# Optimization experiments

Hardware: AMD Instinct MI355X
Metric: run time of the kernel (lower is better)

The kernel has to match this reference:

```python
import jax, jax.numpy as jnp
import numpy as np

SCENE = (128, 128, 8)      # (X, Y, Z) voxel grid
VOXEL_SIZE = 0.4
DOWNSAMPLE_Z = 2
NUM_HEADS = 8
NUM_POINTS = 4
LN_EPS = 1e-5


def _pix2vox(depth, K, E, voxel_origin):
    # depth [1,H,W]; K [1,3,3]; E [1,4,4]; voxel_origin [1,3]
    B, H, W = depth.shape
    gx, gy = jnp.meshgrid(jnp.arange(W, dtype=depth.dtype), jnp.arange(H, dtype=depth.dtype))
    pix = jnp.stack([gx, gy])                              # [2,H,W] -> (u, v) after flip in torch
    d = depth[:, None]                                     # [B,1,H,W]
    p_x = jnp.concatenate([pix[None] * d, d], 1).reshape(B, 3, -1)
    p_c = jnp.linalg.inv(K) @ p_x                          # camera coords [B,3,HW]
    p_c = jnp.concatenate([p_c, jnp.ones_like(p_c[:, :1])], 1)
    p_w = jnp.linalg.inv(E) @ p_c                          # world coords [B,4,HW]
    p_v = (jnp.swapaxes(p_w[:, :3], 1, 2) - voxel_origin[:, None, :]) / VOXEL_SIZE - 0.5
    p_v = p_v.at[..., 2].set(p_v[..., 2] / DOWNSAMPLE_Z)
    return jnp.trunc(p_v).astype(jnp.int32)               # torch .long() truncates toward 0


def _voxel_mask(p_v):
    X, Y, Z = SCENE
    p = p_v[0]                                             # [HW,3] (batch asserted == 1)
    valid = ((p[:, 0] >= 0) & (p[:, 0] < X) & (p[:, 1] >= 0) & (p[:, 1] < Y)
             & (p[:, 2] >= 0) & (p[:, 2] < Z))
    flat = jnp.where(valid, (p[:, 0] * Y + p[:, 1]) * Z + p[:, 2], 0)
    return jnp.zeros(X * Y * Z, dtype=bool).at[flat].max(valid)


def _ms_deform_attn(q, feats, ref, Wv, bv, Woff, boff, Wattw, battw, Wout, bout):
    # q [N,C]; feats: list of [C,Hl,Wl]; ref [N,2] normalized (shared across levels)
    N, C = q.shape
    hd = C // NUM_HEADS
    shapes = [(f.shape[1], f.shape[2]) for f in feats]
    L = len(feats)
    flat = jnp.concatenate([f.reshape(C, -1).T for f in feats], 0)      # [Lsum, C]
    value = (flat @ Wv.T + bv).reshape(-1, NUM_HEADS, hd)               # [Lsum, h, hd]
    off = (q @ Woff.T + boff).reshape(N, NUM_HEADS, L, NUM_POINTS, 2)
    w = jax.nn.softmax((q @ Wattw.T + battw).reshape(N, NUM_HEADS, L * NUM_POINTS), -1)
    w = w.reshape(N, NUM_HEADS, L, NUM_POINTS)
    normalizer = jnp.array([[wl, hl] for (hl, wl) in shapes], dtype=q.dtype)  # (W,H) per level
    loc = ref[:, None, None, None, :] + off / normalizer[None, None, :, None, :]
    h_idx = jnp.arange(NUM_HEADS)[None, :, None]
    out = jnp.zeros((N, NUM_HEADS, hd), q.dtype)
    start = 0
    for lvl, (Hl, Wl) in enumerate(shapes):
        v = value[start:start + Hl * Wl]                   # [Hl*Wl, h, hd]
        start += Hl * Wl
        # grid_sample bilinear, align_corners=False, zero padding
        x = loc[:, :, lvl, :, 0] * Wl - 0.5                # [N,h,P]
        y = loc[:, :, lvl, :, 1] * Hl - 0.5
        x0 = jnp.floor(x); y0 = jnp.floor(y)
        lx = x - x0; ly = y - y0
        x0i = x0.astype(jnp.int32); y0i = y0.astype(jnp.int32)
        samp = jnp.zeros((N, NUM_HEADS, NUM_POINTS, hd), q.dtype)
        for dy, dx, wgt in ((0, 0, (1 - lx) * (1 - ly)), (0, 1, lx * (1 - ly)),
                            (1, 0, (1 - lx) * ly), (1, 1, lx * ly)):
            xi = x0i + dx; yi = y0i + dy
            ok = (xi >= 0) & (xi < Wl) & (yi >= 0) & (yi < Hl)
            idx = jnp.where(ok, yi * Wl + xi, 0)
            g = v[idx, h_idx]                              # [N,h,P,hd] per-head gather
            samp = samp + g * (wgt * ok)[..., None]
        out = out + jnp.einsum('nhp,nhpd->nhd', w[:, :, lvl], samp)
    return out.reshape(N, C) @ Wout.T + bout


def _forward(scene_embed, feat0, feat1, feat2, depth, K, E, voxel_origin, ref_pix,
             Wv, bv, Woff, boff, Wattw, battw, Wout, bout, ln_g, ln_b):
    X, Y, Z = SCENE
    mask = _voxel_mask(_pix2vox(depth, K, E, voxel_origin))             # [N] bool
    q = scene_embed[0]                                                  # [N,C]
    attn = _ms_deform_attn(q, [feat0[0], feat1[0], feat2[0]], ref_pix[0],
                           Wv, bv, Woff, boff, Wattw, battw, Wout, bout)
    h = q + attn                                                        # residual (MSDeformAttn identity)
    mu = jnp.mean(h, -1, keepdims=True)
    var = jnp.mean((h - mu) ** 2, -1, keepdims=True)
    h = (h - mu) / jnp.sqrt(var + LN_EPS) * ln_g + ln_b                 # post-norm
    out = jnp.where(mask[:, None], h, q)                                # index_fov_back_to_voxels
    return out.T.reshape(1, -1, X, Y, Z)                                # nlc -> nchw [1,C,X,Y,Z]


def setup_inputs() -> dict:
    key = jax.random.key(0)
    ks = jax.random.split(key, 12)
    X, Y, Z = SCENE
    N = X * Y * Z
    C = 128
    H, W = 192, 640
    s = 0.02
    scene_embed = jax.random.normal(ks[0], (1, N, C), jnp.float32)
    feat0 = jax.random.normal(ks[1], (1, C, 48, 160), jnp.float32)
    feat1 = jax.random.normal(ks[2], (1, C, 24, 80), jnp.float32)
    feat2 = jax.random.normal(ks[3], (1, C, 12, 40), jnp.float32)
    depth = jax.random.uniform(ks[4], (1, H, W), jnp.float32, 1.0, 40.0)
    K = jnp.array([[[552.55, 0.0, 320.0], [0.0, 552.55, 96.0], [0.0, 0.0, 1.0]]], jnp.float32)
    E = jnp.eye(4, dtype=jnp.float32)[None]
    voxel_origin = jnp.array([[-25.6, -3.2, 0.0]], jnp.float32)
    ref_pix = jax.random.uniform(ks[5], (1, N, 2), jnp.float32)
    return {
        'scene_embed': scene_embed, 'feat0': feat0, 'feat1': feat1, 'feat2': feat2,
        'depth': depth, 'K': K, 'E': E, 'voxel_origin': voxel_origin, 'ref_pix': ref_pix,
        'Wv': jax.random.normal(ks[6], (C, C), jnp.float32) * s,
        'bv': jnp.zeros((C,), jnp.float32),
        'Woff': jax.random.normal(ks[7], (NUM_HEADS * 3 * NUM_POINTS * 2, C), jnp.float32) * s,
        'boff': jnp.zeros((NUM_HEADS * 3 * NUM_POINTS * 2,), jnp.float32),
        'Wattw': jax.random.normal(ks[8], (NUM_HEADS * 3 * NUM_POINTS, C), jnp.float32) * s,
        'battw': jnp.zeros((NUM_HEADS * 3 * NUM_POINTS,), jnp.float32),
        'Wout': jax.random.normal(ks[9], (C, C), jnp.float32) * s,
        'bout': jnp.zeros((C,), jnp.float32),
        'ln_g': jnp.ones((C,), jnp.float32),
        'ln_b': jnp.zeros((C,), jnp.float32),
    }


def reference(scene_embed, feat0, feat1, feat2, depth, K, E, voxel_origin, ref_pix,
              Wv, bv, Woff, boff, Wattw, battw, Wout, bout, ln_g, ln_b):
    return _forward(scene_embed, feat0, feat1, feat2, depth, K, E, voxel_origin, ref_pix,
                    Wv, bv, Woff, boff, Wattw, battw, Wout, bout, ln_g, ln_b)
```

## Files before the change

kernel.cpp:

```cpp
#include <hip/hip_runtime.h>
#include <hip/hip_bf16.h>
#include <stdint.h>

#define XS 128
#define YS 128
#define ZS 8
#define NQ (XS*YS*ZS)
#define CDIM 128
#define NH 8
#define HD 16
#define DH 192
#define DW 640
#define NPIX (DH*DW)
#define NVPIX 10080

typedef float f32x4 __attribute__((ext_vector_type(4)));
typedef short s16x8 __attribute__((ext_vector_type(8)));
typedef unsigned int u32x4 __attribute__((ext_vector_type(4)));

__device__ __forceinline__ float b2f(unsigned short u){
    union { unsigned int i; float f; } v; v.i = ((unsigned int)u) << 16; return v.f;
}
__device__ __forceinline__ unsigned short f2b(float f){
    __hip_bfloat16 h = __float2bfloat16(f);
    return *reinterpret_cast<unsigned short*>(&h);
}
__device__ __forceinline__ float blo(unsigned int u){
    union { unsigned int i; float f; } v; v.i = u << 16; return v.f;
}
__device__ __forceinline__ float bhi(unsigned int u){
    union { unsigned int i; float f; } v; v.i = u & 0xffff0000u; return v.f;
}

__global__ __launch_bounds__(256)
void prep_kernel(int nW, int nVal,
                 const float* __restrict__ Woff,
                 const float* __restrict__ Wattw,
                 const float* __restrict__ Wout,
                 unsigned short* __restrict__ Wbf,
                 const float* __restrict__ f0,
                 const float* __restrict__ f1,
                 const float* __restrict__ f2,
                 const float* __restrict__ Wv,
                 const float* __restrict__ bv,
                 unsigned short* __restrict__ value,
                 const float* __restrict__ depth,
                 const float* __restrict__ K,
                 const float* __restrict__ E,
                 const float* __restrict__ vorigin,
                 unsigned char* __restrict__ mask){
    __shared__ __align__(16) unsigned char smem[16384];
    const int t = threadIdx.x;

    if ((int)blockIdx.x < nW){
        int idx = blockIdx.x*256 + t;
        if (idx < 24576)      Wbf[idx] = f2b(Woff[idx]);
        else if (idx < 36864) Wbf[idx] = f2b(Wattw[idx-24576]);
        else if (idx < 40960) Wbf[idx] = 0;
        else if (idx < 57344) Wbf[idx] = f2b(Wout[idx-40960]);
    } else if ((int)blockIdx.x < nW + nVal){
        const int half = t >> 7, tt = t & 127;
        const int p0 = (blockIdx.x - nW)*8 + half*4;
        float (*fl)[4] = (float(*)[4])(smem + half*2048);
        const float* src; int hw, lp;
        if (p0 < 7680)      { src=f0; hw=7680; lp=p0; }
        else if (p0 < 9600) { src=f1; hw=1920; lp=p0-7680; }
        else                { src=f2; hw=480;  lp=p0-9600; }
        float4 v = *(const float4*)(src + tt*hw + lp);
        fl[tt][0]=v.x; fl[tt][1]=v.y; fl[tt][2]=v.z; fl[tt][3]=v.w;
        __syncthreads();
        float bb = bv[tt];
        float acc[4] = {bb,bb,bb,bb};
        const float4* wrow = (const float4*)(Wv + tt*CDIM);
        #pragma unroll 8
        for (int kc=0; kc<32; ++kc){
            float4 w = wrow[kc];
            #pragma unroll
            for (int u=0;u<4;u++){
                float wu = (u==0)?w.x:(u==1)?w.y:(u==2)?w.z:w.w;
                float4 fv = *(const float4*)fl[kc*4+u];
                acc[0] += fv.x*wu; acc[1] += fv.y*wu; acc[2] += fv.z*wu; acc[3] += fv.w*wu;
            }
        }
        const int hh = tt >> 4, cc = tt & 15;
        #pragma unroll
        for (int i=0;i<4;i++)
            value[((size_t)hh*NVPIX + (size_t)(p0+i))*HD + cc] = f2b(acc[i]);
    } else {
        double* invs = (double*)smem;
        if (t == 0){
            double k[3][3], e[4][4];
            for (int i=0;i<9;i++)  k[i/3][i%3] = (double)K[i];
            for (int i=0;i<16;i++) e[i/4][i%4] = (double)E[i];
            double det = k[0][0]*(k[1][1]*k[2][2]-k[1][2]*k[2][1])
                       - k[0][1]*(k[1][0]*k[2][2]-k[1][2]*k[2][0])
                       + k[0][2]*(k[1][0]*k[2][1]-k[1][1]*k[2][0]);
            double id = 1.0/det;
            invs[0]=(k[1][1]*k[2][2]-k[1][2]*k[2][1])*id;
            invs[1]=(k[0][2]*k[2][1]-k[0][1]*k[2][2])*id;
            invs[2]=(k[0][1]*k[1][2]-k[0][2]*k[1][1])*id;
            invs[3]=(k[1][2]*k[2][0]-k[1][0]*k[2][2])*id;
            invs[4]=(k[0][0]*k[2][2]-k[0][2]*k[2][0])*id;
            invs[5]=(k[0][2]*k[1][0]-k[0][0]*k[1][2])*id;
            invs[6]=(k[1][0]*k[2][1]-k[1][1]*k[2][0])*id;
            invs[7]=(k[0][1]*k[2][0]-k[0][0]*k[2][1])*id;
            invs[8]=(k[0][0]*k[1][1]-k[0][1]*k[1][0])*id;
            double a[4][8];
            for (int i=0;i<4;i++){ for(int j=0;j<4;j++){ a[i][j]=e[i][j]; a[i][4+j]=(i==j)?1.0:0.0; } }
            for (int c=0;c<4;c++){
                int piv=c; double best=fabs(a[c][c]);
                for (int r=c+1;r<4;r++){ double v=fabs(a[r][c]); if (v>best){best=v;piv=r;} }
                if (piv!=c){ for (int j=0;j<8;j++){ double tmp=a[c][j]; a[c][j]=a[piv][j]; a[piv][j]=tmp; } }
                double pv = 1.0/a[c][c];
                for (int j=0;j<8;j++) a[c][j]*=pv;
                for (int r=0;r<4;r++){
                    if (r==c) continue;
                    double f=a[r][c];
                    for(int j=0;j<8;j++) a[r][j]-=f*a[c][j];
                }
            }
            for (int i=0;i<12;i++) invs[9+i] = a[i/4][4 + (i%4)];
        }
        __syncthreads();
        int tid = ((int)blockIdx.x - nW - nVal)*256 + t;
        if (tid >= NPIX) return;
        int gx = tid % DW, gy = tid / DW;
        double d  = (double)depth[tid];
        double X0 = (double)gx * d, X1 = (double)gy * d, X2 = d;
        double c0 = invs[0]*X0 + invs[1]*X1 + invs[2]*X2;
        double c1 = invs[3]*X0 + invs[4]*X1 + invs[5]*X2;
        double c2 = invs[6]*X0 + invs[7]*X1 + invs[8]*X2;
        const double* iE = invs + 9;
        double w0 = iE[0]*c0 + iE[1]*c1 + iE[2]*c2  + iE[3];
        double w1 = iE[4]*c0 + iE[5]*c1 + iE[6]*c2  + iE[7];
        double w2 = iE[8]*c0 + iE[9]*c1 + iE[10]*c2 + iE[11];
        double v0 = (w0-(double)vorigin[0])/0.4 - 0.5;
        double v1 = (w1-(double)vorigin[1])/0.4 - 0.5;
        double v2 = ((w2-(double)vorigin[2])/0.4 - 0.5) / 2.0;
        int xi = (int)v0, yi = (int)v1, zi = (int)v2;
        if (xi>=0 && xi<XS && yi>=0 && yi<YS && zi>=0 && zi<ZS)
            mask[(xi*YS + yi)*ZS + zi] = 1;
    }
}

__global__ __launch_bounds__(256, 2)
void attn_fused(const float* __restrict__ q_in,
                const float* __restrict__ refpix,
                const unsigned short* __restrict__ Wbf,
                const float* __restrict__ boff,
                const float* __restrict__ battw,
                const unsigned short* __restrict__ value,
                const unsigned short* __restrict__ WoutBf,
                const float* __restrict__ bout,
                const float* __restrict__ lng,
                const float* __restrict__ lnb,
                const unsigned char* __restrict__ mask,
                float* __restrict__ dout){
    const int nq0 = blockIdx.x * 32;
    const int t = threadIdx.x;
    __shared__ __align__(16) unsigned char smem[36384];
    unsigned short* Ob    = (unsigned short*)smem;
    unsigned char*  qbfB  = smem + 18432;
    unsigned char*  descB = smem + 18432;
    float*          out2  = (float*)(smem + 18432);
    unsigned char*  obfB  = smem + 30720;
    float*          bias  = (float*)(smem + 34816);
    float*          rp_s  = (float*)(smem + 35968);
    unsigned char*  mask_s= smem + 36224;
    float*          wredp = (float*)(smem + 36256);

    #pragma unroll
    for (int i=0;i<4;i++){
        int idx = t + i*256;
        int row = idx >> 5, c4 = idx & 31;
        float4 qv = ((const float4*)(q_in + (size_t)(nq0+row)*CDIM))[c4];
        unsigned int pk0 = (unsigned int)f2b(qv.x) | ((unsigned int)f2b(qv.y)<<16);
        unsigned int pk1 = (unsigned int)f2b(qv.z) | ((unsigned int)f2b(qv.w)<<16);
        unsigned int bo = ((unsigned int)(row*256 + c4*8)) ^ (unsigned int)((row&7)<<4);
        *(unsigned int*)(qbfB + bo)     = pk0;
        *(unsigned int*)(qbfB + bo + 4) = pk1;
    }
    for (int i=t;i<288;i+=256) bias[i] = (i<192)? boff[i] : battw[i-192];
    ((unsigned int*)obfB)[512 + t] = 0;
    ((unsigned int*)obfB)[768 + t] = 0;
    if (t < 64) rp_s[t] = refpix[nq0*2 + t];
    if (t < 32) mask_s[t] = mask[nq0 + t];
    __syncthreads();

    {
        const int w = t >> 6, lane = t & 63, lr = lane & 15, lg = lane >> 4;
        const int nt0 = w*5;
        f32x4 acc[5][2];
        #pragma unroll
        for (int j=0;j<5;j++){ acc[j][0]=(f32x4){0,0,0,0}; acc[j][1]=(f32x4){0,0,0,0}; }
        #pragma unroll
        for (int ks=0; ks<4; ++ks){
            s16x8 bf[2];
            #pragma unroll
            for (int qt=0;qt<2;qt++){
                int qrow = qt*16 + lr;
                unsigned int bo = ((unsigned int)(qrow*256 + ks*64 + lg*16)) ^ (unsigned int)((qrow&7)<<4);
                bf[qt] = *(const s16x8*)(qbfB + bo);
            }
            const unsigned short* wp = Wbf + (size_t)(nt0*16 + lr)*CDIM + ks*32 + lg*8;
            #pragma unroll
            for (int j=0;j<5;++j){
                s16x8 af = *(const s16x8*)(wp + j*16*CDIM);
                acc[j][0] = __builtin_amdgcn_mfma_f32_16x16x32_bf16(af, bf[0], acc[j][0], 0, 0, 0);
                acc[j][1] = __builtin_amdgcn_mfma_f32_16x16x32_bf16(af, bf[1], acc[j][1], 0, 0, 0);
            }
        }
        #pragma unroll
        for (int j=0;j<5;++j){
            int nt = nt0 + j;
            if (nt < 18){
                #pragma unroll
                for (int qt=0;qt<2;qt++){
                    int q = qt*16 + lr;
                    int base = (q>>3)*2304 + (q&7);
                    #pragma unroll
                    for (int r=0;r<4;++r){
                        int f = nt*16 + lg*4 + r;
                        Ob[base + f*8] = f2b(acc[j][qt][r] + bias[f]);
                    }
                }
            }
        }
    }
    __syncthreads();

    {
        int q = t >> 3, h = t & 7;
        unsigned short* p = Ob + (q>>3)*2304 + (192 + h*12)*8 + (q&7);
        float e[12]; float m = -1e30f;
        #pragma unroll
        for (int i=0;i<12;i++){ e[i] = b2f(p[i*8]); m = fmaxf(m, e[i]); }
        float s = 0.f;
        #pragma unroll
        for (int i=0;i<12;i++){ e[i] = __expf(e[i]-m); s += e[i]; }
        float is = 1.f/s;
        #pragma unroll
        for (int i=0;i<12;i++) p[i*8] = f2b(e[i]*is);
    }
    __syncthreads();

    for (int sr = 0; sr < 4; ++sr){
        const unsigned short* raw = Ob + sr*2304;
        const int nsr = nq0 + sr*8;

        for (int idx = t; idx < 768; idx += 256){
            int q = idx & 7, hp = idx >> 3;
            int lp = hp % 12;
            float fw, fh; int Wl, Hl, st;
            if (lp < 4)      { fw=160.f; fh=48.f; Wl=160; Hl=48; st=0; }
            else if (lp < 8) { fw=80.f;  fh=24.f; Wl=80;  Hl=24; st=7680; }
            else             { fw=40.f;  fh=12.f; Wl=40;  Hl=12; st=9600; }
            float offx = b2f(raw[(hp*2)*8 + q]);
            float offy = b2f(raw[(hp*2+1)*8 + q]);
            float aw   = b2f(raw[(192+hp)*8 + q]);
            float x = rp_s[(sr*8+q)*2+0]*fw - 0.5f + offx;
            float y = rp_s[(sr*8+q)*2+1]*fh - 0.5f + offy;
            float x0f = floorf(x), y0f = floorf(y);
            float lx = x-x0f, ly = y-y0f;
            int x0 = (int)x0f, y0 = (int)y0f;
            bool x0ok = (x0>=0)&&(x0<Wl), x1ok=(x0+1>=0)&&(x0+1<Wl);
            bool y0ok = (y0>=0)&&(y0<Hl), y1ok=(y0+1>=0)&&(y0+1<Hl);
            float w00 = (x0ok&&y0ok)? (1.f-lx)*(1.f-ly)*aw : 0.f;
            float w01 = (x1ok&&y0ok)? lx*(1.f-ly)*aw       : 0.f;
            float w10 = (x0ok&&y1ok)? (1.f-lx)*ly*aw       : 0.f;
            float w11 = (x1ok&&y1ok)? lx*ly*aw             : 0.f;
            int yc0 = min(max(y0,0),Hl-1), yc1 = min(max(y0+1,0),Hl-1);
            int xc0 = min(max(x0,0),Wl-1), xc1 = min(max(x0+1,0),Wl-1);
            unsigned int rb0 = (unsigned int)(st + yc0*Wl), rb1 = (unsigned int)(st + yc1*Wl);
            uint4 d;
            d.x = (rb0+(unsigned int)xc0) | ((rb0+(unsigned int)xc1)<<16);
            d.y = (rb1+(unsigned int)xc0) | ((rb1+(unsigned int)xc1)<<16);
            d.z = (unsigned int)f2b(w00) | ((unsigned int)f2b(w01)<<16);
            d.w = (unsigned int)f2b(w10) | ((unsigned int)f2b(w11)<<16);
            *(uint4*)(descB + (((unsigned int)(idx ^ ((idx>>5)&7)))<<4)) = d;
        }
        __syncthreads();

        float qv[4];
        {
            const int r = t & 127, qb = t >> 7;
            #pragma unroll
            for (int qi4=0;qi4<4;qi4++)
                qv[qi4] = q_in[(size_t)(nsr + qb*4 + qi4)*CDIM + r];
        }

        {
            const int cs  = t & 1;
            const int cp2 = (t >> 1) & 1;
            const int hs  = (t >> 2) & 7;
            const int qq  = t >> 5;
            const unsigned int vbase = (unsigned int)hs*(NVPIX*HD*2) + (unsigned int)cp2*16;
            const char* vb = (const char*)value;
            float a8[8] = {0.f,0.f,0.f,0.f,0.f,0.f,0.f,0.f};
            #pragma unroll
            for (int lp=0; lp<12; ++lp){
                int idx = (hs*12+lp)*8 + qq;
                uint4 d = *(const uint4*)(descB + (((unsigned int)(idx ^ ((idx>>5)&7)))<<4));
                unsigned int pidx = cs ? d.y : d.x;
                unsigned int wpk  = cs ? d.w : d.z;
                unsigned int oa = vbase + ((pidx & 0xffffu)<<5);
                unsigned int ob = vbase + ((pidx >> 16)<<5);
                u32x4 ua = *(const u32x4*)(vb + oa);
                u32x4 ub = *(const u32x4*)(vb + ob);
                float wa = blo(wpk), wb = bhi(wpk);
                #pragma unroll
                for (int j=0;j<4;j++){
                    a8[2*j]   += blo(ua[j])*wa + blo(ub[j])*wb;
                    a8[2*j+1] += bhi(ua[j])*wa + bhi(ub[j])*wb;
                }
            }
            #pragma unroll
            for (int j=0;j<8;j++) a8[j] += __shfl_xor(a8[j], 1, 64);
            if (cs == 0){
                u32x4 pk;
                pk[0] = (unsigned int)f2b(a8[0]) | ((unsigned int)f2b(a8[1])<<16);
                pk[1] = (unsigned int)f2b(a8[2]) | ((unsigned int)f2b(a8[3])<<16);
                pk[2] = (unsigned int)f2b(a8[4]) | ((unsigned int)f2b(a8[5])<<16);
                pk[3] = (unsigned int)f2b(a8[6]) | ((unsigned int)f2b(a8[7])<<16);
                unsigned int bo = ((unsigned int)(qq*256 + hs*32 + cp2*16)) ^ (unsigned int)((qq&7)<<4);
                *(u32x4*)(obfB + bo) = pk;
            }
        }
        __syncthreads();

        {
            const int w = t >> 6, lane = t & 63, lr = lane & 15, lg = lane >> 4;
            f32x4 a0 = (f32x4){0.f,0.f,0.f,0.f};
            f32x4 a1 = (f32x4){0.f,0.f,0.f,0.f};
            #pragma unroll
            for (int ks=0; ks<4; ++ks){
                unsigned int bo = (unsigned int)(lr*256 + ks*64 + lg*16) ^ (unsigned int)((lr&7)<<4);
                s16x8 bfrag = *(const s16x8*)(obfB + bo);
                const unsigned short* wp = WoutBf + (size_t)(w*32 + lr)*CDIM + ks*32 + lg*8;
                s16x8 af0 = *(const s16x8*)(wp);
                s16x8 af1 = *(const s16x8*)(wp + 16*CDIM);
                a0 = __builtin_amdgcn_mfma_f32_16x16x32_bf16(af0, bfrag, a0, 0, 0, 0);
                a1 = __builtin_amdgcn_mfma_f32_16x16x32_bf16(af1, bfrag, a1, 0, 0, 0);
            }
            if (lr < 8){
                int f0 = w*32 + lg*4;
                float4 b0 = *(const float4*)(bout + f0);
                float4 b1 = *(const float4*)(bout + f0 + 16);
                float4 v0, v1;
                v0.x = a0[0]+b0.x; v0.y = a0[1]+b0.y; v0.z = a0[2]+b0.z; v0.w = a0[3]+b0.w;
                v1.x = a1[0]+b1.x; v1.y = a1[1]+b1.y; v1.z = a1[2]+b1.z; v1.w = a1[3]+b1.w;
                *(float4*)(out2 + lr*CDIM + f0)      = v0;
                *(float4*)(out2 + lr*CDIM + f0 + 16) = v1;
            }
        }
        __syncthreads();

        {
            const int r = t & 127;
            const int qb = t >> 7;
            const int wv = t >> 6;
            float hv[4], s1[4], s2[4];
            #pragma unroll
            for (int qi4=0;qi4<4;qi4++){
                hv[qi4] = qv[qi4] + out2[(qb*4+qi4)*CDIM + r];
                s1[qi4] = hv[qi4];
                s2[qi4] = hv[qi4]*hv[qi4];
            }
            #pragma unroll
            for (int off=32; off>0; off>>=1){
                #pragma unroll
                for (int qi4=0;qi4<4;qi4++){
                    s1[qi4] += __shfl_xor(s1[qi4], off, 64);
                    s2[qi4] += __shfl_xor(s2[qi4], off, 64);
                }
            }
            if ((t&63)==0){
                #pragma unroll
                for (int qi4=0;qi4<4;qi4++){
                    wredp[0*16 + wv*4 + qi4] = s1[qi4];
                    wredp[1*16 + wv*4 + qi4] = s2[qi4];
                }
            }
            __syncthreads();

            float res[4];
            const float g = lng[r], b = lnb[r];
            #pragma unroll
            for (int qi4=0;qi4<4;qi4++){
                float mu  = (wredp[0*16 + (qb*2)*4 + qi4] + wredp[0*16 + (qb*2+1)*4 + qi4]) * (1.f/128.f);
                float msq = (wredp[1*16 + (qb*2)*4 + qi4] + wredp[1*16 + (qb*2+1)*4 + qi4]) * (1.f/128.f);
                float var = msq - mu*mu;
                float nv  = (hv[qi4]-mu) * __frsqrt_rn(var + 1e-5f) * g + b;
                res[qi4] = mask_s[sr*8 + qb*4+qi4] ? nv : qv[qi4];
            }
            float4 o; o.x=res[0]; o.y=res[1]; o.z=res[2]; o.w=res[3];
            *(float4*)(dout + (size_t)r*NQ + nsr + qb*4) = o;
        }
        __syncthreads();
    }
}

extern "C" void kernel_launch(void* const* d_in, const int* in_sizes, int n_in,
                              void* d_out, int out_size, void* d_ws, size_t ws_size,
                              hipStream_t stream){
    const float* scene  = (const float*)d_in[0];
    const float* f0     = (const float*)d_in[1];
    const float* f1     = (const float*)d_in[2];
    const float* f2     = (const float*)d_in[3];
    const float* depth  = (const float*)d_in[4];
    const float* K      = (const float*)d_in[5];
    const float* E      = (const float*)d_in[6];
    const float* vorig  = (const float*)d_in[7];
    const float* refpix = (const float*)d_in[8];
    const float* Wv     = (const float*)d_in[9];
    const float* bv     = (const float*)d_in[10];
    const float* Woff   = (const float*)d_in[11];
    const float* boff   = (const float*)d_in[12];
    const float* Wattw  = (const float*)d_in[13];
    const float* battw  = (const float*)d_in[14];
    const float* Wout   = (const float*)d_in[15];
    const float* bout   = (const float*)d_in[16];
    const float* lng    = (const float*)d_in[17];
    const float* lnb    = (const float*)d_in[18];

    char* ws = (char*)d_ws;
    unsigned char*  mask   = (unsigned char*)(ws + 512);
    unsigned short* value  = (unsigned short*)(ws + 512 + 131072);
    unsigned short* Wbf    = (unsigned short*)(ws + 512 + 131072 + 2580480);
    unsigned short* WoutBf = Wbf + 40960;

    hipMemsetAsync(mask, 0, NQ, stream);

    int nW    = 57344/256;
    int nVal  = NVPIX/8;
    int nMask = (NPIX+255)/256;
    prep_kernel<<<nW + nVal + nMask, 256, 0, stream>>>(
        nW, nVal, Woff, Wattw, Wout, Wbf,
        f0, f1, f2, Wv, bv, value,
        depth, K, E, vorig, mask);
    attn_fused<<<NQ/32, 256, 0, stream>>>(scene, refpix, Wbf, boff, battw, value,
                                          WoutBf, bout, lng, lnb, mask,
                                          (float*)d_out);
}
```

Baseline: 402.1 us.

## Halve queries per block and remap bilinear gather threads for higher occupancy

The fused attention kernel now handles 16 queries per block instead of 32, doubling the grid, shrinking shared memory, and raising the launch-bounds occupancy hint from 2 to 6 blocks per CU. The first MFMA projection drops its second query tile, which cuts accumulator registers. The value-gather stage is remapped so each thread loads 4-byte channel pairs for two queries across all four bilinear corners, replacing 16-byte loads plus a shuffle reduction. This aims at more latency hiding for the random gathers, at the cost of narrower memory accesses and more per-block overhead such as reloading the weights.

```diff
diff --git a/kernel.cpp b/kernel.cpp
--- a/kernel.cpp
+++ b/kernel.cpp
@@ -16,7 +16,6 @@
 
 typedef float f32x4 __attribute__((ext_vector_type(4)));
 typedef short s16x8 __attribute__((ext_vector_type(8)));
-typedef unsigned int u32x4 __attribute__((ext_vector_type(4)));
 
 __device__ __forceinline__ float b2f(unsigned short u){
     union { unsigned int i; float f; } v; v.i = ((unsigned int)u) << 16; return v.f;
@@ -143,7 +142,7 @@
     }
 }
 
-__global__ __launch_bounds__(256, 2)
+__global__ __launch_bounds__(256, 6)
 void attn_fused(const float* __restrict__ q_in,
                 const float* __restrict__ refpix,
                 const unsigned short* __restrict__ Wbf,
@@ -156,21 +155,21 @@
                 const float* __restrict__ lnb,
                 const unsigned char* __restrict__ mask,
                 float* __restrict__ dout){
-    const int nq0 = blockIdx.x * 32;
+    const int nq0 = blockIdx.x * 16;
     const int t = threadIdx.x;
-    __shared__ __align__(16) unsigned char smem[36384];
+    __shared__ __align__(16) unsigned char smem[27024];
     unsigned short* Ob    = (unsigned short*)smem;
-    unsigned char*  qbfB  = smem + 18432;
-    unsigned char*  descB = smem + 18432;
-    float*          out2  = (float*)(smem + 18432);
-    unsigned char*  obfB  = smem + 30720;
-    float*          bias  = (float*)(smem + 34816);
-    float*          rp_s  = (float*)(smem + 35968);
-    unsigned char*  mask_s= smem + 36224;
-    float*          wredp = (float*)(smem + 36256);
+    unsigned char*  qbfB  = smem + 9216;
+    unsigned char*  descB = smem + 9216;
+    float*          out2  = (float*)(smem + 9216);
+    unsigned char*  obfB  = smem + 21504;
+    float*          bias  = (float*)(smem + 25600);
+    float*          rp_s  = (float*)(smem + 26752);
+    unsigned char*  mask_s= smem + 26880;
+    float*          wredp = (float*)(smem + 26896);
 
     #pragma unroll
-    for (int i=0;i<4;i++){
+    for (int i=0;i<2;i++){
         int idx = t + i*256;
         int row = idx >> 5, c4 = idx & 31;
         float4 qv = ((const float4*)(q_in + (size_t)(nq0+row)*CDIM))[c4];
@@ -183,53 +182,43 @@
     for (int i=t;i<288;i+=256) bias[i] = (i<192)? boff[i] : battw[i-192];
     ((unsigned int*)obfB)[512 + t] = 0;
     ((unsigned int*)obfB)[768 + t] = 0;
-    if (t < 64) rp_s[t] = refpix[nq0*2 + t];
-    if (t < 32) mask_s[t] = mask[nq0 + t];
+    if (t < 32) rp_s[t] = refpix[nq0*2 + t];
+    if (t < 16) mask_s[t] = mask[nq0 + t];
     __syncthreads();
 
     {
         const int w = t >> 6, lane = t & 63, lr = lane & 15, lg = lane >> 4;
         const int nt0 = w*5;
-        f32x4 acc[5][2];
-        #pragma unroll
-        for (int j=0;j<5;j++){ acc[j][0]=(f32x4){0,0,0,0}; acc[j][1]=(f32x4){0,0,0,0}; }
+        f32x4 acc[5];
+        #pragma unroll
+        for (int j=0;j<5;j++) acc[j]=(f32x4){0,0,0,0};
         #pragma unroll
         for (int ks=0; ks<4; ++ks){
-            s16x8 bf[2];
-            #pragma unroll
-            for (int qt=0;qt<2;qt++){
-                int qrow = qt*16 + lr;
-                unsigned int bo = ((unsigned int)(qrow*256 + ks*64 + lg*16)) ^ (unsigned int)((qrow&7)<<4);
-                bf[qt] = *(const s16x8*)(qbfB + bo);
-            }
+            unsigned int bo = ((unsigned int)(lr*256 + ks*64 + lg*16)) ^ (unsigned int)((lr&7)<<4);
+            s16x8 bfrag = *(const s16x8*)(qbfB + bo);
             const unsigned short* wp = Wbf + (size_t)(nt0*16 + lr)*CDIM + ks*32 + lg*8;
             #pragma unroll
             for (int j=0;j<5;++j){
                 s16x8 af = *(const s16x8*)(wp + j*16*CDIM);
-                acc[j][0] = __builtin_amdgcn_mfma_f32_16x16x32_bf16(af, bf[0], acc[j][0], 0, 0, 0);
-                acc[j][1] = __builtin_amdgcn_mfma_f32_16x16x32_bf16(af, bf[1], acc[j][1], 0, 0, 0);
+                acc[j] = __builtin_amdgcn_mfma_f32_16x16x32_bf16(af, bfrag, acc[j], 0, 0, 0);
             }
         }
         #pragma unroll
         for (int j=0;j<5;++j){
             int nt = nt0 + j;
             if (nt < 18){
+                int base = (lr>>3)*2304 + (lr&7);
                 #pragma unroll
-                for (int qt=0;qt<2;qt++){
-                    int q = qt*16 + lr;
-                    int base = (q>>3)*2304 + (q&7);
-                    #pragma unroll
-                    for (int r=0;r<4;++r){
-                        int f = nt*16 + lg*4 + r;
-                        Ob[base + f*8] = f2b(acc[j][qt][r] + bias[f]);
-                    }
+                for (int r=0;r<4;++r){
+                    int f = nt*16 + lg*4 + r;
+                    Ob[base + f*8] = f2b(acc[j][r] + bias[f]);
                 }
             }
         }
     }
     __syncthreads();
 
-    {
+    if (t < 128){
         int q = t >> 3, h = t & 7;
         unsigned short* p = Ob + (q>>3)*2304 + (192 + h*12)*8 + (q&7);
         float e[12]; float m = -1e30f;
@@ -244,7 +233,7 @@
     }
     __syncthreads();
 
-    for (int sr = 0; sr < 4; ++sr){
+    for (int sr = 0; sr < 2; ++sr){
         const unsigned short* raw = Ob + sr*2304;
         const int nsr = nq0 + sr*8;
 
@@ -290,41 +279,38 @@
         }
 
         {
-            const int cs  = t & 1;
-            const int cp2 = (t >> 1) & 1;
-            const int hs  = (t >> 2) & 7;
-            const int qq  = t >> 5;
-            const unsigned int vbase = (unsigned int)hs*(NVPIX*HD*2) + (unsigned int)cp2*16;
+            const int cp = t & 7, hs = (t>>3) & 7, qgs = t >> 6;
+            const unsigned int vbase = (unsigned int)hs*(NVPIX*HD*2) + (unsigned int)cp*4;
             const char* vb = (const char*)value;
-            float a8[8] = {0.f,0.f,0.f,0.f,0.f,0.f,0.f,0.f};
+            float av0x=0.f, av0y=0.f, av1x=0.f, av1y=0.f;
             #pragma unroll
             for (int lp=0; lp<12; ++lp){
-                int idx = (hs*12+lp)*8 + qq;
-                uint4 d = *(const uint4*)(descB + (((unsigned int)(idx ^ ((idx>>5)&7)))<<4));
-                unsigned int pidx = cs ? d.y : d.x;
-                unsigned int wpk  = cs ? d.w : d.z;
-                unsigned int oa = vbase + ((pidx & 0xffffu)<<5);
-                unsigned int ob = vbase + ((pidx >> 16)<<5);
-                u32x4 ua = *(const u32x4*)(vb + oa);
-                u32x4 ub = *(const u32x4*)(vb + ob);
-                float wa = blo(wpk), wb = bhi(wpk);
                 #pragma unroll
-                for (int j=0;j<4;j++){
-                    a8[2*j]   += blo(ua[j])*wa + blo(ub[j])*wb;
-                    a8[2*j+1] += bhi(ua[j])*wa + bhi(ub[j])*wb;
+                for (int qi2=0; qi2<2; ++qi2){
+                    int idx = (hs*12+lp)*8 + qgs*2 + qi2;
+                    uint4 d = *(const uint4*)(descB + (((unsigned int)(idx ^ ((idx>>5)&7)))<<4));
+                    unsigned int o00 = vbase + ((d.x & 0xffffu)<<5);
+                    unsigned int o01 = vbase + ((d.x >> 16)<<5);
+                    unsigned int o10 = vbase + ((d.y & 0xffffu)<<5);
+                    unsigned int o11 = vbase + ((d.y >> 16)<<5);
+                    unsigned int u00 = *(const unsigned int*)(vb + o00);
+                    unsigned int u01 = *(const unsigned int*)(vb + o01);
+                    unsigned int u10 = *(const unsigned int*)(vb + o10);
+                    unsigned int u11 = *(const unsigned int*)(vb + o11);
+                    float w00 = blo(d.z), w01 = bhi(d.z), w10 = blo(d.w), w11 = bhi(d.w);
+                    float sx = blo(u00)*w00 + blo(u01)*w01 + blo(u10)*w10 + blo(u11)*w11;
+                    float sy = bhi(u00)*w00 + bhi(u01)*w01 + bhi(u10)*w10 + bhi(u11)*w11;
+                    if (qi2 == 0){ av0x += sx; av0y += sy; }
+                    else         { av1x += sx; av1y += sy; }
                 }
             }
-            #pragma unroll
-            for (int j=0;j<8;j++) a8[j] += __shfl_xor(a8[j], 1, 64);
-            if (cs == 0){
-                u32x4 pk;
-                pk[0] = (unsigned int)f2b(a8[0]) | ((unsigned int)f2b(a8[1])<<16);
-                pk[1] = (unsigned int)f2b(a8[2]) | ((unsigned int)f2b(a8[3])<<16);
-                pk[2] = (unsigned int)f2b(a8[4]) | ((unsigned int)f2b(a8[5])<<16);
-                pk[3] = (unsigned int)f2b(a8[6]) | ((unsigned int)f2b(a8[7])<<16);
-                unsigned int bo = ((unsigned int)(qq*256 + hs*32 + cp2*16)) ^ (unsigned int)((qq&7)<<4);
-                *(u32x4*)(obfB + bo) = pk;
-            }
+            const int q0q = qgs*2;
+            unsigned int pk0 = (unsigned int)f2b(av0x) | ((unsigned int)f2b(av0y)<<16);
+            unsigned int pk1 = (unsigned int)f2b(av1x) | ((unsigned int)f2b(av1y)<<16);
+            unsigned int bo0 = (unsigned int)(q0q*256 + hs*32 + cp*4)     ^ (unsigned int)((q0q&7)<<4);
+            unsigned int bo1 = (unsigned int)((q0q+1)*256 + hs*32 + cp*4) ^ (unsigned int)(((q0q+1)&7)<<4);
+            *(unsigned int*)(obfB + bo0) = pk0;
+            *(unsigned int*)(obfB + bo1) = pk1;
         }
         __syncthreads();
 
@@ -438,7 +424,7 @@
         nW, nVal, Woff, Wattw, Wout, Wbf,
         f0, f1, f2, Wv, bv, value,
         depth, K, E, vorig, mask);
-    attn_fused<<<NQ/32, 256, 0, stream>>>(scene, refpix, Wbf, boff, battw, value,
+    attn_fused<<<NQ/16, 256, 0, stream>>>(scene, refpix, Wbf, boff, battw, value,
                                           WoutBf, bout, lng, lnb, mask,
                                           (float*)d_out);
 }
```

Measured after the change: 594.6 us. +47.9%, slower.
